# Performance work log

Hardware: AMD Instinct MI355X
Metric: run time of the kernel (lower is better)

Reference implementation:

```python
import jax, jax.numpy as jnp
import numpy as np

C = 64            # x_channel (d_model)
D = 2 * C         # d_inner (expand=2)
N = C // 2        # d_state
K = 4             # scan directions
R = -(-C // 16)   # dt_rank = ceil(d_model/16)
Bsz, H, W = 2, 48, 48
EPS = 1e-5


def setup_inputs() -> dict:
    key = jax.random.key(0)
    ks = jax.random.split(key, 8)
    g = lambda k, shp, s: jax.random.normal(k, shp, dtype=jnp.float32) * s
    return {
        "fufea1": g(ks[0], (Bsz, C, H, W), 1.0),
        "ln_g": jnp.ones((C,), jnp.float32),
        "ln_b": jnp.zeros((C,), jnp.float32),
        "in_proj_w": g(ks[1], (2 * D, C), C ** -0.5),
        "conv_w": g(ks[2], (D, 1, 3, 3), 1.0 / 3.0),   # depthwise 3x3
        "conv_b": g(ks[3], (D,), 0.02),
        "x_proj_w": g(ks[4], (K, R + 2 * N, D), D ** -0.5),
        "dt_w": g(ks[5], (K, D, R), R ** -0.5),
        "dt_b": g(ks[6], (K, D), 0.1),
        "A_logs": jnp.log(jnp.tile(jnp.arange(1, N + 1, dtype=jnp.float32), (K, D, 1))),  # S4D-real init
        "Ds": jnp.ones((K, D), jnp.float32),
        "out_ln_g": jnp.ones((D,), jnp.float32),
        "out_ln_b": jnp.zeros((D,), jnp.float32),
        "out_proj_w": g(ks[7], (C, D), D ** -0.5),
    }


def _layernorm(x, g, b):
    mu = x.mean(-1, keepdims=True)
    var = ((x - mu) ** 2).mean(-1, keepdims=True)
    return (x - mu) * jax.lax.rsqrt(var + EPS) * g + b


def reference(fufea1, ln_g, ln_b, in_proj_w, conv_w, conv_b, x_proj_w,
              dt_w, dt_b, A_logs, Ds, out_ln_g, out_ln_b, out_proj_w):
    B, Cc, Hh, Ww = fufea1.shape
    L = Hh * Ww
    # pre-LN (over channels, channels-last)
    xn = _layernorm(fufea1.transpose(0, 2, 3, 1), ln_g, ln_b)          # (B,H,W,C)
    # SS2D: in_proj -> split x,z
    xz = xn @ in_proj_w.T                                               # (B,H,W,2D)
    x, z = jnp.split(xz, 2, axis=-1)
    x = x.transpose(0, 3, 1, 2)                                         # (B,D,H,W)
    x = jax.lax.conv_general_dilated(x, conv_w, (1, 1), "SAME",
                                     feature_group_count=D,
                                     dimension_numbers=("NCHW", "OIHW", "NCHW"))
    x = jax.nn.silu(x + conv_b[None, :, None, None])
    # 4-direction sequences: row-major, col-major, and their reverses
    x_hw = x.reshape(B, D, L)
    x_wh = x.transpose(0, 1, 3, 2).reshape(B, D, L)
    xs = jnp.stack([x_hw, x_wh], axis=1)                                # (B,2,D,L)
    xs = jnp.concatenate([xs, jnp.flip(xs, axis=-1)], axis=1)           # (B,K,D,L)
    # per-direction projections of dt, B, C
    x_dbl = jnp.einsum("bkdl,kcd->bkcl", xs, x_proj_w)
    dts, Bs, Cs = jnp.split(x_dbl, [R, R + N], axis=2)                  # (B,K,R,L),(B,K,N,L),(B,K,N,L)
    dts = jnp.einsum("bkrl,kdr->bkdl", dts, dt_w)
    delta = jax.nn.softplus(dts + dt_b[None, :, :, None])               # (B,K,D,L)
    A = -jnp.exp(A_logs)                                                # (K,D,N)
    # selective scan over L; carry h: (B,K,D,N)
    u_l = xs.transpose(3, 0, 1, 2)                                      # (L,B,K,D)
    dt_l = delta.transpose(3, 0, 1, 2)
    B_l = Bs.transpose(3, 0, 1, 2)                                      # (L,B,K,N)
    C_l = Cs.transpose(3, 0, 1, 2)

    def step(h, inp):
        u_t, d_t, b_t, c_t = inp
        dA = jnp.exp(d_t[..., None] * A)                                # (B,K,D,N)
        h = dA * h + (d_t * u_t)[..., None] * b_t[:, :, None, :]
        y = jnp.einsum("bkdn,bkn->bkd", h, c_t)
        return h, y

    h0 = jnp.zeros((B, K, D, N), xs.dtype)
    _, ys = jax.lax.scan(step, h0, (u_l, dt_l, B_l, C_l))               # ys: (L,B,K,D)
    out_y = ys.transpose(1, 2, 3, 0) + Ds[None, :, :, None] * xs        # (B,K,D,L)
    # merge the 4 directions back to row-major hw order
    inv_y = jnp.flip(out_y[:, 2:4], axis=-1)                            # (B,2,D,L)
    wh = lambda t: t.reshape(B, D, Ww, Hh).transpose(0, 1, 3, 2).reshape(B, D, L)
    y = out_y[:, 0] + inv_y[:, 0] + wh(out_y[:, 1]) + wh(inv_y[:, 1])   # (B,D,L)
    y = y.transpose(0, 2, 1).reshape(B, Hh, Ww, D)
    y = _layernorm(y, out_ln_g, out_ln_b) * jax.nn.silu(z)
    out = (y @ out_proj_w.T).transpose(0, 3, 1, 2) + fufea1             # residual add
    return out
```

## Files before the change

### kernel.cpp

```cpp
#include <hip/hip_runtime.h>

#define Cc 64
#define Dd 128
#define Nn 32
#define Kk 4
#define Rr 4
#define Bb 2
#define Hh 48
#define Ww 48
#define Ll 2304
#define EPSf 1e-5f
#define LCc 144

#if __has_builtin(__builtin_amdgcn_exp2f)
#define EXP2F __builtin_amdgcn_exp2f
#else
#define EXP2F exp2f
#endif

__device__ __forceinline__ float wsum64(float v) {
  v += __shfl_xor(v, 32);
  v += __shfl_xor(v, 16);
  v += __shfl_xor(v, 8);
  v += __shfl_xor(v, 4);
  v += __shfl_xor(v, 2);
  v += __shfl_xor(v, 1);
  return v;
}

__device__ __forceinline__ float hmax32(float v) {
  v = fmaxf(v, __shfl_xor(v, 1));
  v = fmaxf(v, __shfl_xor(v, 2));
  v = fmaxf(v, __shfl_xor(v, 4));
  v = fmaxf(v, __shfl_xor(v, 8));
  v = fmaxf(v, __shfl_xor(v, 16));
  return v;
}

__device__ __forceinline__ int pixbase(int j, int k) {
  if (k == 0) return j;
  if (k == 2) return Ll - 1 - j;
  if (k == 1) return (j % Hh) * Ww + (j / Hh);
  const int jr = Ll - 1 - j;
  return (jr % Hh) * Ww + (jr / Hh);
}

__global__ __launch_bounds__(256) void k1_ln_inproj(
    const float* __restrict__ x, const float* __restrict__ g,
    const float* __restrict__ bta, const float* __restrict__ Wp,
    float* __restrict__ xin, float* __restrict__ zb)
{
  __shared__ float xS[16][65];
  __shared__ float xnS[16][64];
  const int tid = threadIdx.x;
  const int wv = tid >> 6, lane = tid & 63;
  const int pbase = blockIdx.x * 16;
  const int b = pbase / Ll;
  const int lbase = pbase % Ll;
  {
    const int c = tid >> 2, li0 = (tid & 3) * 4;
    const float4 v4 = *(const float4*)&x[(b * Cc + c) * Ll + lbase + li0];
    xS[li0 + 0][c] = v4.x;
    xS[li0 + 1][c] = v4.y;
    xS[li0 + 2][c] = v4.z;
    xS[li0 + 3][c] = v4.w;
  }
  __syncthreads();
  const float gv = g[lane], bv = bta[lane];
  for (int pi = 0; pi < 4; ++pi) {
    const int p = wv * 4 + pi;
    const float v = xS[p][lane];
    const float mu = wsum64(v) * (1.0f / 64.0f);
    const float dv = v - mu;
    const float var = wsum64(dv * dv) * (1.0f / 64.0f);
    const float rs = rsqrtf(var + EPSf);
    xnS[p][lane] = dv * rs * gv + bv;
  }
  __syncthreads();
  float acc[4][4];
  #pragma unroll
  for (int pi = 0; pi < 4; ++pi)
    #pragma unroll
    for (int m = 0; m < 4; ++m) acc[pi][m] = 0.f;
  const float4* W4 = (const float4*)Wp;
  #pragma unroll 4
  for (int c4 = 0; c4 < 16; ++c4) {
    float4 xn4[4];
    #pragma unroll
    for (int pi = 0; pi < 4; ++pi)
      xn4[pi] = ((const float4*)xnS[wv * 4 + pi])[c4];
    #pragma unroll
    for (int m = 0; m < 4; ++m) {
      const float4 w4 = W4[(lane + 64 * m) * 16 + c4];
      #pragma unroll
      for (int pi = 0; pi < 4; ++pi)
        acc[pi][m] += xn4[pi].x * w4.x + xn4[pi].y * w4.y +
                      xn4[pi].z * w4.z + xn4[pi].w * w4.w;
    }
  }
  #pragma unroll
  for (int pi = 0; pi < 4; ++pi) {
    const int l = lbase + wv * 4 + pi;
    const size_t base = (size_t)(b * Ll + l) * Dd;
    xin[base + lane]      = acc[pi][0];
    xin[base + lane + 64] = acc[pi][1];
    zb[base + lane]       = acc[pi][2];
    zb[base + lane + 64]  = acc[pi][3];
  }
}

__global__ __launch_bounds__(512) void k3_proj(
    const float* __restrict__ xin, const float* __restrict__ cw,
    const float* __restrict__ cb, const float* __restrict__ xpw,
    const float* __restrict__ dtw, const float* __restrict__ dtb,
    float* __restrict__ xc, float2* __restrict__ dd2,
    float* __restrict__ Bm, float* __restrict__ Cm)
{
  __shared__ float xinS[30][128];
  __shared__ float xvS[8][132];
  __shared__ float dtsS[8][16];
  const int t = threadIdx.x;
  const int pb = blockIdx.x * 8;
  const int b = pb / Ll;
  const int lb = pb % Ll;
  const int h0 = lb / Ww, w0 = lb % Ww;
  for (int i = t; i < 960; i += 512) {
    const int j = i >> 5, d4 = i & 31;
    const int r = j / 10, c = j % 10;
    const int hh = h0 + r - 1, ww = w0 + c - 1;
    float4 v = make_float4(0.f, 0.f, 0.f, 0.f);
    if (hh >= 0 && hh < Hh && ww >= 0 && ww < Ww)
      v = *(const float4*)&xin[((size_t)(b * Ll) + hh * Ww + ww) * Dd + d4 * 4];
    *(float4*)&xinS[j][d4 * 4] = v;
  }
  __syncthreads();
  for (int i = t; i < 1024; i += 512) {
    const int pi = i >> 7, d = i & 127;
    float acc = cb[d];
    #pragma unroll
    for (int r = 0; r < 3; ++r)
      #pragma unroll
      for (int c = 0; c < 3; ++c)
        acc += xinS[r * 10 + pi + c][d] * cw[d * 9 + r * 3 + c];
    const float sig = 1.0f / (1.0f + __expf(-acc));
    xvS[pi][d] = acc * sig;
  }
  __syncthreads();
  if (t < 272) {
    const int k = t / 68, c = t % 68;
    const size_t bkL = (size_t)(b * Kk + k) * Ll;
    float acc[8];
    #pragma unroll
    for (int pi = 0; pi < 8; ++pi) acc[pi] = 0.f;
    const float4* w4p = (const float4*)(xpw + (k * 68 + c) * 128);
    for (int d4 = 0; d4 < 32; ++d4) {
      const float4 w4 = w4p[d4];
      #pragma unroll
      for (int pi = 0; pi < 8; ++pi) {
        const float4 x4 = ((const float4*)xvS[pi])[d4];
        acc[pi] += x4.x * w4.x + x4.y * w4.y + x4.z * w4.z + x4.w * w4.w;
      }
    }
    #pragma unroll
    for (int pi = 0; pi < 8; ++pi) {
      const int l0 = lb + pi;
      const int h = l0 / Ww, w = l0 % Ww;
      int lk;
      if      (k == 0) lk = l0;
      else if (k == 1) lk = w * Hh + h;
      else if (k == 2) lk = Ll - 1 - l0;
      else             lk = Ll - 1 - (w * Hh + h);
      if (c < Rr)            dtsS[pi][k * 4 + c] = acc[pi];
      else if (c < Rr + Nn)  Bm[(bkL + lk) * Nn + (c - Rr)] = acc[pi];
      else                   Cm[(bkL + lk) * Nn + (c - Rr - Nn)] = acc[pi];
    }
  } else {
    for (int i = t - 272; i < 1024; i += 240) {
      const int pi = i >> 7, d = i & 127;
      xc[((size_t)(b * Ll) + lb + pi) * Dd + d] = xvS[pi][d];
    }
  }
  __syncthreads();
  {
    const int k = t >> 7, dd = t & 127;
    const float4 dw = *(const float4*)&dtw[(k * Dd + dd) * 4];
    const float biasv = dtb[k * Dd + dd];
    float2* drow = dd2 + ((size_t)((b * Kk + k) * Dd) + dd) * Ll;
    float2 buf[8];
    #pragma unroll
    for (int pi = 0; pi < 8; ++pi) {
      const float a = biasv
          + dtsS[pi][k * 4 + 0] * dw.x + dtsS[pi][k * 4 + 1] * dw.y
          + dtsS[pi][k * 4 + 2] * dw.z + dtsS[pi][k * 4 + 3] * dw.w;
      const float sp = (a > 20.f) ? a : log1pf(__expf(a));
      buf[pi] = make_float2(sp, sp * xvS[pi][dd]);
    }
    float4* f4 = (float4*)(drow + lb);
    #pragma unroll
    for (int j = 0; j < 4; ++j)
      f4[j] = make_float4(buf[2 * j].x, buf[2 * j].y, buf[2 * j + 1].x, buf[2 * j + 1].y);
  }
}

__global__ __launch_bounds__(512) void k4_scan(
    const float2* __restrict__ dd2, const float* __restrict__ Bm,
    const float* __restrict__ Cm, const float* __restrict__ Alogs,
    float* __restrict__ ys)
{
  __shared__ float2 ddS[Ll];
  __shared__ float hcS[16][32];
  __shared__ float sumDS[16];
  __shared__ float cmaxS[16];
  __shared__ float pS[16][8][36];
  const int tid = threadIdx.x;
  const int s = tid >> 5, n = tid & 31;
  const int blk = blockIdx.x;
  const int bk = blk & 7;
  const int d = blk >> 3;
  const int b = bk >> 2, k = bk & 3;
  const float An = -__expf(Alogs[(k * Dd + d) * Nn + n]);
  const float AnE = An * 1.44269504f;
  const size_t bkL = (size_t)(b * Kk + k) * Ll;
  const float2* dP = dd2 + ((size_t)((b * Kk + k) * Dd) + d) * Ll;
  const float* bP = Bm + bkL * Nn + n;
  const float* cP = Cm + bkL * Nn + n;
  const int lbeg = s * LCc;
  float* yD = ys + ((size_t)((b * Kk + k) * Dd) + d) * Ll;
  const int pstr = (k == 0) ? 1 : (k == 1) ? Ww : (k == 2) ? -1 : -Ww;
  const int rrow = n & 7, qtr = n >> 3;

  {
    const float4* src = (const float4*)dP;
    float4* dst = (float4*)ddS;
    #pragma unroll
    for (int i = 0; i < 3; ++i) {
      const int idx = tid + i * 512;
      if (idx < Ll / 2) dst[idx] = src[idx];
    }
  }
  __syncthreads();

  float h = 0.f, sumD = 0.f, cmx = 0.f;
  {
    const float* bl = bP + (size_t)lbeg * Nn;
    const float* cl = cP + (size_t)lbeg * Nn;
    float b0 = bl[0], b1 = bl[Nn], b2 = bl[2 * Nn], b3 = bl[3 * Nn];
    float c0 = cl[0], c1 = cl[Nn], c2 = cl[2 * Nn], c3 = cl[3 * Nn];
    int pb = pixbase(lbeg, k);
    float2 q0 = ddS[pb], q1 = ddS[pb + pstr], q2 = ddS[pb + 2 * pstr], q3 = ddS[pb + 3 * pstr];
    for (int t8 = 0; t8 < LCc / 8; ++t8) {
      const int j0n = lbeg + t8 * 8 + 8;
      const int pbn = pixbase(j0n <= Ll - 8 ? j0n : Ll - 8, k);
      #pragma unroll
      for (int half = 0; half < 2; ++half) {
        bl += 4 * Nn; cl += 4 * Nn;
        const int gb = (half == 0) ? pb + 4 * pstr : pbn;
        const float2 qn0 = ddS[gb], qn1 = ddS[gb + pstr],
                     qn2 = ddS[gb + 2 * pstr], qn3 = ddS[gb + 3 * pstr];
        const float b0n = bl[0], b1n = bl[Nn], b2n = bl[2 * Nn], b3n = bl[3 * Nn];
        const float c0n = cl[0], c1n = cl[Nn], c2n = cl[2 * Nn], c3n = cl[3 * Nn];
        h = EXP2F(q0.x * AnE) * h + q0.y * b0; pS[s][half * 4 + 0][n] = h * c0;
        h = EXP2F(q1.x * AnE) * h + q1.y * b1; pS[s][half * 4 + 1][n] = h * c1;
        h = EXP2F(q2.x * AnE) * h + q2.y * b2; pS[s][half * 4 + 2][n] = h * c2;
        h = EXP2F(q3.x * AnE) * h + q3.y * b3; pS[s][half * 4 + 3][n] = h * c3;
        sumD += (q0.x + q1.x) + (q2.x + q3.x);
        cmx = fmaxf(cmx, fmaxf(fmaxf(fabsf(c0), fabsf(c1)),
                               fmaxf(fabsf(c2), fabsf(c3))));
        q0 = qn0; q1 = qn1; q2 = qn2; q3 = qn3;
        b0 = b0n; b1 = b1n; b2 = b2n; b3 = b3n;
        c0 = c0n; c1 = c1n; c2 = c2n; c3 = c3n;
      }
      const float4 a4 = *(const float4*)&pS[s][rrow][qtr * 8];
      const float4 d4v = *(const float4*)&pS[s][rrow][qtr * 8 + 4];
      float sum = ((a4.x + a4.y) + (a4.z + a4.w)) + ((d4v.x + d4v.y) + (d4v.z + d4v.w));
      sum += __shfl_xor(sum, 8);
      sum += __shfl_xor(sum, 16);
      if (n < 8) yD[pb + n * pstr] = sum;
      pb = pbn;
    }
  }
  hcS[s][n] = h;
  const float cmxAll = hmax32(cmx);
  if (n == 0) { sumDS[s] = sumD; cmaxS[s] = cmxAll; }
  __syncthreads();
  if (tid < 32) {
    float carry = 0.f;
    #pragma unroll
    for (int s2 = 0; s2 < 16; ++s2) {
      const float hend = hcS[s2][tid];
      hcS[s2][tid] = carry;
      carry = EXP2F(AnE * sumDS[s2]) * carry + hend;
    }
  }
  __syncthreads();
  const float carry = hcS[s][n];
  const float mc = hmax32(fabsf(carry));
  const float AmaxE = hmax32(AnE);
  const float Pstop = log2f(mc * cmaxS[s] * 3.2e6f) / (-AmaxE);
  {
    float hc = carry, P = 0.f;
    const float* cl = cP + (size_t)lbeg * Nn;
    for (int t8 = 0; t8 < LCc / 8; ++t8) {
      if (!(P < Pstop)) break;
      const int pb = pixbase(lbeg + t8 * 8, k);
      #pragma unroll
      for (int half = 0; half < 2; ++half) {
        const int gb = pb + half * 4 * pstr;
        const float2 qq0 = ddS[gb], qq1 = ddS[gb + pstr],
                     qq2 = ddS[gb + 2 * pstr], qq3 = ddS[gb + 3 * pstr];
        hc *= EXP2F(qq0.x * AnE); pS[s][half * 4 + 0][n] = hc * cl[0];
        hc *= EXP2F(qq1.x * AnE); pS[s][half * 4 + 1][n] = hc * cl[Nn];
        hc *= EXP2F(qq2.x * AnE); pS[s][half * 4 + 2][n] = hc * cl[2 * Nn];
        hc *= EXP2F(qq3.x * AnE); pS[s][half * 4 + 3][n] = hc * cl[3 * Nn];
        P += (qq0.x + qq1.x) + (qq2.x + qq3.x);
        cl += 4 * Nn;
      }
      const float4 a4 = *(const float4*)&pS[s][rrow][qtr * 8];
      const float4 d4v = *(const float4*)&pS[s][rrow][qtr * 8 + 4];
      float sum = ((a4.x + a4.y) + (a4.z + a4.w)) + ((d4v.x + d4v.y) + (d4v.z + d4v.w));
      sum += __shfl_xor(sum, 8);
      sum += __shfl_xor(sum, 16);
      if (n < 8) yD[pb + n * pstr] += sum;
    }
  }
}

__global__ __launch_bounds__(256) void k5_merge(
    const float* __restrict__ ys, const float* __restrict__ zb,
    const float* __restrict__ og, const float* __restrict__ ob,
    const float* __restrict__ Wo, const float* __restrict__ resid,
    const float* __restrict__ xc, const float* __restrict__ DsP,
    float* __restrict__ out)
{
  __shared__ float ysS[16][132];
  __shared__ float xcS[16][128];
  __shared__ float tS[16][128];
  __shared__ float oS[64][17];
  const int tid = threadIdx.x;
  const int wv = tid >> 6, lane = tid & 63;
  const int pbase = blockIdx.x * 16;
  const int b = pbase / Ll;
  const int lbase = pbase % Ll;
  {
    const int li0 = (tid & 3) * 4, dh = tid >> 2;
    #pragma unroll
    for (int it = 0; it < 2; ++it) {
      const int d = dh + 64 * it;
      float4 acc = make_float4(0.f, 0.f, 0.f, 0.f);
      #pragma unroll
      for (int k = 0; k < 4; ++k) {
        const float4 v = *(const float4*)&ys[((size_t)(b * Kk + k) * Dd + d) * Ll + lbase + li0];
        acc.x += v.x; acc.y += v.y; acc.z += v.z; acc.w += v.w;
      }
      ysS[li0 + 0][d] = acc.x; ysS[li0 + 1][d] = acc.y;
      ysS[li0 + 2][d] = acc.z; ysS[li0 + 3][d] = acc.w;
    }
  }
  {
    const int p = tid >> 4, q = tid & 15;
    const float4* src = (const float4*)&xc[((size_t)(b * Ll) + lbase + p) * Dd];
    ((float4*)xcS[p])[q]      = src[q];
    ((float4*)xcS[p])[q + 16] = src[q + 16];
  }
  float sDs[2];
  #pragma unroll
  for (int m = 0; m < 2; ++m) {
    const int dch = lane + 64 * m;
    sDs[m] = DsP[dch] + DsP[Dd + dch] + DsP[2 * Dd + dch] + DsP[3 * Dd + dch];
  }
  __syncthreads();
  for (int pi = 0; pi < 4; ++pi) {
    const int p = wv * 4 + pi;
    const int l0 = lbase + p;
    float tv[2];
    #pragma unroll
    for (int m = 0; m < 2; ++m) {
      const int dch = lane + 64 * m;
      tv[m] = ysS[p][dch] + sDs[m] * xcS[p][dch];
    }
    const float mu = wsum64(tv[0] + tv[1]) * (1.0f / 128.0f);
    const float q = wsum64((tv[0] - mu) * (tv[0] - mu) +
                           (tv[1] - mu) * (tv[1] - mu)) * (1.0f / 128.0f);
    const float rs = rsqrtf(q + EPSf);
    #pragma unroll
    for (int m = 0; m < 2; ++m) {
      const int dch = lane + 64 * m;
      const float zz = zb[(size_t)(b * Ll + l0) * Dd + dch];
      const float sig = 1.0f / (1.0f + __expf(-zz));
      tS[p][dch] = ((tv[m] - mu) * rs * og[dch] + ob[dch]) * (zz * sig);
    }
  }
  __syncthreads();
  float acc[4] = {0.f, 0.f, 0.f, 0.f};
  const float4* W4 = (const float4*)Wo;
  for (int d4 = 0; d4 < 32; ++d4) {
    const float4 w4 = W4[lane * 32 + d4];
    #pragma unroll
    for (int pi = 0; pi < 4; ++pi) {
      const float4 t4 = ((const float4*)tS[wv * 4 + pi])[d4];
      acc[pi] += t4.x * w4.x + t4.y * w4.y + t4.z * w4.z + t4.w * w4.w;
    }
  }
  #pragma unroll
  for (int pi = 0; pi < 4; ++pi) oS[lane][wv * 4 + pi] = acc[pi];
  __syncthreads();
  const int c = tid >> 2, off = (tid & 3) * 4;
  const size_t obase = (size_t)(b * Cc + c) * Ll + lbase + off;
  const float4 r4 = *(const float4*)(resid + obase);
  float4 o4;
  o4.x = oS[c][off + 0] + r4.x;
  o4.y = oS[c][off + 1] + r4.y;
  o4.z = oS[c][off + 2] + r4.z;
  o4.w = oS[c][off + 3] + r4.w;
  *(float4*)(out + obase) = o4;
}

extern "C" void kernel_launch(void* const* d_in, const int* in_sizes, int n_in,
                              void* d_out, int out_size, void* d_ws, size_t ws_size,
                              hipStream_t stream)
{
  (void)in_sizes; (void)n_in; (void)out_size; (void)ws_size;
  const float* fufea1     = (const float*)d_in[0];
  const float* ln_g       = (const float*)d_in[1];
  const float* ln_b       = (const float*)d_in[2];
  const float* in_proj_w  = (const float*)d_in[3];
  const float* conv_w     = (const float*)d_in[4];
  const float* conv_b     = (const float*)d_in[5];
  const float* x_proj_w   = (const float*)d_in[6];
  const float* dt_w       = (const float*)d_in[7];
  const float* dt_b       = (const float*)d_in[8];
  const float* A_logs     = (const float*)d_in[9];
  const float* Ds         = (const float*)d_in[10];
  const float* out_ln_g   = (const float*)d_in[11];
  const float* out_ln_b   = (const float*)d_in[12];
  const float* out_proj_w = (const float*)d_in[13];

  float* ws = (float*)d_ws;
  float2* dd2 = (float2*)ws;
  float* Bm   = ws + 4718592;
  float* Cm   = ws + 5308416;
  float* zb   = ws + 5898240;
  float* xc   = ws + 6488064;
  float* ysb  = ws + 7077888;
  float* xin  = ws + 7077888;

  k1_ln_inproj<<<288, 256, 0, stream>>>(fufea1, ln_g, ln_b, in_proj_w, xin, zb);
  k3_proj<<<576, 512, 0, stream>>>(xin, conv_w, conv_b, x_proj_w, dt_w, dt_b,
                                   xc, dd2, Bm, Cm);
  k4_scan<<<1024, 512, 0, stream>>>(dd2, Bm, Cm, A_logs, ysb);
  k5_merge<<<288, 256, 0, stream>>>(ysb, zb, out_ln_g, out_ln_b, out_proj_w, fufea1,
                                    xc, Ds, (float*)d_out);
}
```

Before: 186.6 us.

## Fuse LayerNorm and in_proj into conv/projection kernel with halo recompute

Removes the separate LN+in_proj kernel and computes LayerNorm and the x-half of in_proj inside the conv/x_proj kernel for a 3x10 halo tile, writing z only for the 8 interior pixels. This drops one kernel launch and the global round-trip of the x-half activation buffer. The cost is recomputing the projection for halo pixels (about 3.75x redundant work on that half) and strided, uncoalesced per-channel input reads.

```diff
diff --git a/kernel.cpp b/kernel.cpp
--- a/kernel.cpp
+++ b/kernel.cpp
@@ -45,77 +45,17 @@
   return (jr % Hh) * Ww + (jr / Hh);
 }
 
-__global__ __launch_bounds__(256) void k1_ln_inproj(
+__global__ __launch_bounds__(512) void k3_proj(
     const float* __restrict__ x, const float* __restrict__ g,
     const float* __restrict__ bta, const float* __restrict__ Wp,
-    float* __restrict__ xin, float* __restrict__ zb)
-{
-  __shared__ float xS[16][65];
-  __shared__ float xnS[16][64];
-  const int tid = threadIdx.x;
-  const int wv = tid >> 6, lane = tid & 63;
-  const int pbase = blockIdx.x * 16;
-  const int b = pbase / Ll;
-  const int lbase = pbase % Ll;
-  {
-    const int c = tid >> 2, li0 = (tid & 3) * 4;
-    const float4 v4 = *(const float4*)&x[(b * Cc + c) * Ll + lbase + li0];
-    xS[li0 + 0][c] = v4.x;
-    xS[li0 + 1][c] = v4.y;
-    xS[li0 + 2][c] = v4.z;
-    xS[li0 + 3][c] = v4.w;
-  }
-  __syncthreads();
-  const float gv = g[lane], bv = bta[lane];
-  for (int pi = 0; pi < 4; ++pi) {
-    const int p = wv * 4 + pi;
-    const float v = xS[p][lane];
-    const float mu = wsum64(v) * (1.0f / 64.0f);
-    const float dv = v - mu;
-    const float var = wsum64(dv * dv) * (1.0f / 64.0f);
-    const float rs = rsqrtf(var + EPSf);
-    xnS[p][lane] = dv * rs * gv + bv;
-  }
-  __syncthreads();
-  float acc[4][4];
-  #pragma unroll
-  for (int pi = 0; pi < 4; ++pi)
-    #pragma unroll
-    for (int m = 0; m < 4; ++m) acc[pi][m] = 0.f;
-  const float4* W4 = (const float4*)Wp;
-  #pragma unroll 4
-  for (int c4 = 0; c4 < 16; ++c4) {
-    float4 xn4[4];
-    #pragma unroll
-    for (int pi = 0; pi < 4; ++pi)
-      xn4[pi] = ((const float4*)xnS[wv * 4 + pi])[c4];
-    #pragma unroll
-    for (int m = 0; m < 4; ++m) {
-      const float4 w4 = W4[(lane + 64 * m) * 16 + c4];
-      #pragma unroll
-      for (int pi = 0; pi < 4; ++pi)
-        acc[pi][m] += xn4[pi].x * w4.x + xn4[pi].y * w4.y +
-                      xn4[pi].z * w4.z + xn4[pi].w * w4.w;
-    }
-  }
-  #pragma unroll
-  for (int pi = 0; pi < 4; ++pi) {
-    const int l = lbase + wv * 4 + pi;
-    const size_t base = (size_t)(b * Ll + l) * Dd;
-    xin[base + lane]      = acc[pi][0];
-    xin[base + lane + 64] = acc[pi][1];
-    zb[base + lane]       = acc[pi][2];
-    zb[base + lane + 64]  = acc[pi][3];
-  }
-}
-
-__global__ __launch_bounds__(512) void k3_proj(
-    const float* __restrict__ xin, const float* __restrict__ cw,
-    const float* __restrict__ cb, const float* __restrict__ xpw,
-    const float* __restrict__ dtw, const float* __restrict__ dtb,
+    const float* __restrict__ cw, const float* __restrict__ cb,
+    const float* __restrict__ xpw, const float* __restrict__ dtw,
+    const float* __restrict__ dtb, float* __restrict__ zb,
     float* __restrict__ xc, float2* __restrict__ dd2,
     float* __restrict__ Bm, float* __restrict__ Cm)
 {
+  __shared__ float xS[30][65];
+  __shared__ float xnS[30][64];
   __shared__ float xinS[30][128];
   __shared__ float xvS[8][132];
   __shared__ float dtsS[8][16];
@@ -124,14 +64,70 @@
   const int b = pb / Ll;
   const int lb = pb % Ll;
   const int h0 = lb / Ww, w0 = lb % Ww;
-  for (int i = t; i < 960; i += 512) {
-    const int j = i >> 5, d4 = i & 31;
-    const int r = j / 10, c = j % 10;
-    const int hh = h0 + r - 1, ww = w0 + c - 1;
-    float4 v = make_float4(0.f, 0.f, 0.f, 0.f);
+  for (int idx = t; idx < 1920; idx += 512) {
+    const int c = idx / 30, j = idx % 30;
+    const int r = j / 10, col = j % 10;
+    const int hh = h0 + r - 1, ww = w0 + col - 1;
+    float v = 0.f;
     if (hh >= 0 && hh < Hh && ww >= 0 && ww < Ww)
-      v = *(const float4*)&xin[((size_t)(b * Ll) + hh * Ww + ww) * Dd + d4 * 4];
-    *(float4*)&xinS[j][d4 * 4] = v;
+      v = x[(b * Cc + c) * Ll + hh * Ww + ww];
+    xS[j][c] = v;
+  }
+  __syncthreads();
+  {
+    const int wv = t >> 6, lane = t & 63;
+    const float gv = g[lane], bv = bta[lane];
+    for (int pi = 0; pi < 4; ++pi) {
+      const int p = wv * 4 + pi;
+      if (p < 30) {
+        const float v = xS[p][lane];
+        const float mu = wsum64(v) * (1.0f / 64.0f);
+        const float dv = v - mu;
+        const float var = wsum64(dv * dv) * (1.0f / 64.0f);
+        const float rs = rsqrtf(var + EPSf);
+        xnS[p][lane] = dv * rs * gv + bv;
+      }
+    }
+  }
+  __syncthreads();
+  {
+    const int d = t & 127, pg = t >> 7;
+    float acc[8] = {0.f, 0.f, 0.f, 0.f, 0.f, 0.f, 0.f, 0.f};
+    const float4* Wr = (const float4*)(Wp + d * Cc);
+    for (int c4 = 0; c4 < 16; ++c4) {
+      const float4 w4 = Wr[c4];
+      #pragma unroll
+      for (int i = 0; i < 8; ++i) {
+        const int j = pg * 8 + i;
+        if (j < 30) {
+          const float4 xn4 = ((const float4*)xnS[j])[c4];
+          acc[i] += xn4.x * w4.x + xn4.y * w4.y + xn4.z * w4.z + xn4.w * w4.w;
+        }
+      }
+    }
+    #pragma unroll
+    for (int i = 0; i < 8; ++i) {
+      const int j = pg * 8 + i;
+      if (j < 30) {
+        const int r = j / 10, col = j % 10;
+        const int hh = h0 + r - 1, ww = w0 + col - 1;
+        const bool ok = (hh >= 0 && hh < Hh && ww >= 0 && ww < Ww);
+        xinS[j][d] = ok ? acc[i] : 0.f;
+      }
+    }
+    const float4* Wz = (const float4*)(Wp + (Dd + d) * Cc);
+    float accz[2] = {0.f, 0.f};
+    for (int c4 = 0; c4 < 16; ++c4) {
+      const float4 w4 = Wz[c4];
+      #pragma unroll
+      for (int i = 0; i < 2; ++i) {
+        const float4 xn4 = ((const float4*)xnS[11 + pg * 2 + i])[c4];
+        accz[i] += xn4.x * w4.x + xn4.y * w4.y + xn4.z * w4.z + xn4.w * w4.w;
+      }
+    }
+    #pragma unroll
+    for (int i = 0; i < 2; ++i)
+      zb[((size_t)(b * Ll) + lb + pg * 2 + i) * Dd + d] = accz[i];
   }
   __syncthreads();
   for (int i = t; i < 1024; i += 512) {
@@ -442,11 +438,9 @@
   float* zb   = ws + 5898240;
   float* xc   = ws + 6488064;
   float* ysb  = ws + 7077888;
-  float* xin  = ws + 7077888;
-
-  k1_ln_inproj<<<288, 256, 0, stream>>>(fufea1, ln_g, ln_b, in_proj_w, xin, zb);
-  k3_proj<<<576, 512, 0, stream>>>(xin, conv_w, conv_b, x_proj_w, dt_w, dt_b,
-                                   xc, dd2, Bm, Cm);
+
+  k3_proj<<<576, 512, 0, stream>>>(fufea1, ln_g, ln_b, in_proj_w, conv_w, conv_b,
+                                   x_proj_w, dt_w, dt_b, zb, xc, dd2, Bm, Cm);
   k4_scan<<<1024, 512, 0, stream>>>(dd2, Bm, Cm, A_logs, ysb);
   k5_merge<<<288, 256, 0, stream>>>(ysb, zb, out_ln_g, out_ln_b, out_proj_w, fufea1,
                                     xc, Ds, (float*)d_out);
```

Measured after the change: 196.5 us. 5.3% more time.

## Process two d-channels per scan block to reuse B/C loads

Applied to the files above, without the earlier changes.

Each scan block now handles two adjacent inner channels, loading both channels' delta/u rows into shared memory and running two interleaved recurrences. The B and C values read from global memory are shared between the two channels, which halves that traffic and gives each thread two independent dependency chains for more instruction-level parallelism. The cost is half as many blocks (512), roughly double the shared memory per block and more registers, so occupancy may drop. The early-exit in the carry-correction pass now runs until both channels reach their stop threshold.

```diff
diff --git a/kernel.cpp b/kernel.cpp
--- a/kernel.cpp
+++ b/kernel.cpp
@@ -207,47 +207,53 @@
     const float* __restrict__ Cm, const float* __restrict__ Alogs,
     float* __restrict__ ys)
 {
-  __shared__ float2 ddS[Ll];
-  __shared__ float hcS[16][32];
-  __shared__ float sumDS[16];
+  __shared__ float2 ddS[2][Ll];
+  __shared__ float hcS[2][16][32];
+  __shared__ float sumDS[2][16];
   __shared__ float cmaxS[16];
-  __shared__ float pS[16][8][36];
+  __shared__ float pSA[16][8][36];
+  __shared__ float pSB[16][8][36];
   const int tid = threadIdx.x;
   const int s = tid >> 5, n = tid & 31;
   const int blk = blockIdx.x;
   const int bk = blk & 7;
-  const int d = blk >> 3;
+  const int dp = blk >> 3;
+  const int d0 = dp * 2;
   const int b = bk >> 2, k = bk & 3;
-  const float An = -__expf(Alogs[(k * Dd + d) * Nn + n]);
-  const float AnE = An * 1.44269504f;
+  const float AnE0 = -__expf(Alogs[(k * Dd + d0) * Nn + n]) * 1.44269504f;
+  const float AnE1 = -__expf(Alogs[(k * Dd + d0 + 1) * Nn + n]) * 1.44269504f;
   const size_t bkL = (size_t)(b * Kk + k) * Ll;
-  const float2* dP = dd2 + ((size_t)((b * Kk + k) * Dd) + d) * Ll;
+  const float2* dP0 = dd2 + ((size_t)((b * Kk + k) * Dd) + d0) * Ll;
   const float* bP = Bm + bkL * Nn + n;
   const float* cP = Cm + bkL * Nn + n;
   const int lbeg = s * LCc;
-  float* yD = ys + ((size_t)((b * Kk + k) * Dd) + d) * Ll;
+  float* yD0 = ys + ((size_t)((b * Kk + k) * Dd) + d0) * Ll;
+  float* yD1 = yD0 + Ll;
   const int pstr = (k == 0) ? 1 : (k == 1) ? Ww : (k == 2) ? -1 : -Ww;
   const int rrow = n & 7, qtr = n >> 3;
 
   {
-    const float4* src = (const float4*)dP;
+    const float4* src = (const float4*)dP0;
     float4* dst = (float4*)ddS;
     #pragma unroll
-    for (int i = 0; i < 3; ++i) {
+    for (int i = 0; i < 5; ++i) {
       const int idx = tid + i * 512;
-      if (idx < Ll / 2) dst[idx] = src[idx];
-    }
-  }
-  __syncthreads();
-
-  float h = 0.f, sumD = 0.f, cmx = 0.f;
+      if (idx < Ll) dst[idx] = src[idx];
+    }
+  }
+  __syncthreads();
+
+  float h0 = 0.f, h1 = 0.f, sD0 = 0.f, sD1 = 0.f, cmx = 0.f;
   {
     const float* bl = bP + (size_t)lbeg * Nn;
     const float* cl = cP + (size_t)lbeg * Nn;
     float b0 = bl[0], b1 = bl[Nn], b2 = bl[2 * Nn], b3 = bl[3 * Nn];
     float c0 = cl[0], c1 = cl[Nn], c2 = cl[2 * Nn], c3 = cl[3 * Nn];
     int pb = pixbase(lbeg, k);
-    float2 q0 = ddS[pb], q1 = ddS[pb + pstr], q2 = ddS[pb + 2 * pstr], q3 = ddS[pb + 3 * pstr];
+    float2 qa0 = ddS[0][pb], qa1 = ddS[0][pb + pstr],
+           qa2 = ddS[0][pb + 2 * pstr], qa3 = ddS[0][pb + 3 * pstr];
+    float2 qb0 = ddS[1][pb], qb1 = ddS[1][pb + pstr],
+           qb2 = ddS[1][pb + 2 * pstr], qb3 = ddS[1][pb + 3 * pstr];
     for (int t8 = 0; t8 < LCc / 8; ++t8) {
       const int j0n = lbeg + t8 * 8 + 8;
       const int pbn = pixbase(j0n <= Ll - 8 ? j0n : Ll - 8, k);
@@ -255,72 +261,111 @@
       for (int half = 0; half < 2; ++half) {
         bl += 4 * Nn; cl += 4 * Nn;
         const int gb = (half == 0) ? pb + 4 * pstr : pbn;
-        const float2 qn0 = ddS[gb], qn1 = ddS[gb + pstr],
-                     qn2 = ddS[gb + 2 * pstr], qn3 = ddS[gb + 3 * pstr];
+        const float2 na0 = ddS[0][gb], na1 = ddS[0][gb + pstr],
+                     na2 = ddS[0][gb + 2 * pstr], na3 = ddS[0][gb + 3 * pstr];
+        const float2 nb0 = ddS[1][gb], nb1 = ddS[1][gb + pstr],
+                     nb2 = ddS[1][gb + 2 * pstr], nb3 = ddS[1][gb + 3 * pstr];
         const float b0n = bl[0], b1n = bl[Nn], b2n = bl[2 * Nn], b3n = bl[3 * Nn];
         const float c0n = cl[0], c1n = cl[Nn], c2n = cl[2 * Nn], c3n = cl[3 * Nn];
-        h = EXP2F(q0.x * AnE) * h + q0.y * b0; pS[s][half * 4 + 0][n] = h * c0;
-        h = EXP2F(q1.x * AnE) * h + q1.y * b1; pS[s][half * 4 + 1][n] = h * c1;
-        h = EXP2F(q2.x * AnE) * h + q2.y * b2; pS[s][half * 4 + 2][n] = h * c2;
-        h = EXP2F(q3.x * AnE) * h + q3.y * b3; pS[s][half * 4 + 3][n] = h * c3;
-        sumD += (q0.x + q1.x) + (q2.x + q3.x);
+        h0 = EXP2F(qa0.x * AnE0) * h0 + qa0.y * b0; pSA[s][half * 4 + 0][n] = h0 * c0;
+        h1 = EXP2F(qb0.x * AnE1) * h1 + qb0.y * b0; pSB[s][half * 4 + 0][n] = h1 * c0;
+        h0 = EXP2F(qa1.x * AnE0) * h0 + qa1.y * b1; pSA[s][half * 4 + 1][n] = h0 * c1;
+        h1 = EXP2F(qb1.x * AnE1) * h1 + qb1.y * b1; pSB[s][half * 4 + 1][n] = h1 * c1;
+        h0 = EXP2F(qa2.x * AnE0) * h0 + qa2.y * b2; pSA[s][half * 4 + 2][n] = h0 * c2;
+        h1 = EXP2F(qb2.x * AnE1) * h1 + qb2.y * b2; pSB[s][half * 4 + 2][n] = h1 * c2;
+        h0 = EXP2F(qa3.x * AnE0) * h0 + qa3.y * b3; pSA[s][half * 4 + 3][n] = h0 * c3;
+        h1 = EXP2F(qb3.x * AnE1) * h1 + qb3.y * b3; pSB[s][half * 4 + 3][n] = h1 * c3;
+        sD0 += (qa0.x + qa1.x) + (qa2.x + qa3.x);
+        sD1 += (qb0.x + qb1.x) + (qb2.x + qb3.x);
         cmx = fmaxf(cmx, fmaxf(fmaxf(fabsf(c0), fabsf(c1)),
                                fmaxf(fabsf(c2), fabsf(c3))));
-        q0 = qn0; q1 = qn1; q2 = qn2; q3 = qn3;
+        qa0 = na0; qa1 = na1; qa2 = na2; qa3 = na3;
+        qb0 = nb0; qb1 = nb1; qb2 = nb2; qb3 = nb3;
         b0 = b0n; b1 = b1n; b2 = b2n; b3 = b3n;
         c0 = c0n; c1 = c1n; c2 = c2n; c3 = c3n;
       }
-      const float4 a4 = *(const float4*)&pS[s][rrow][qtr * 8];
-      const float4 d4v = *(const float4*)&pS[s][rrow][qtr * 8 + 4];
-      float sum = ((a4.x + a4.y) + (a4.z + a4.w)) + ((d4v.x + d4v.y) + (d4v.z + d4v.w));
-      sum += __shfl_xor(sum, 8);
-      sum += __shfl_xor(sum, 16);
-      if (n < 8) yD[pb + n * pstr] = sum;
+      {
+        const float4 a4 = *(const float4*)&pSA[s][rrow][qtr * 8];
+        const float4 d4v = *(const float4*)&pSA[s][rrow][qtr * 8 + 4];
+        float sumA = ((a4.x + a4.y) + (a4.z + a4.w)) + ((d4v.x + d4v.y) + (d4v.z + d4v.w));
+        const float4 e4 = *(const float4*)&pSB[s][rrow][qtr * 8];
+        const float4 f4 = *(const float4*)&pSB[s][rrow][qtr * 8 + 4];
+        float sumB = ((e4.x + e4.y) + (e4.z + e4.w)) + ((f4.x + f4.y) + (f4.z + f4.w));
+        sumA += __shfl_xor(sumA, 8);
+        sumB += __shfl_xor(sumB, 8);
+        sumA += __shfl_xor(sumA, 16);
+        sumB += __shfl_xor(sumB, 16);
+        if (n < 8) {
+          yD0[pb + n * pstr] = sumA;
+          yD1[pb + n * pstr] = sumB;
+        }
+      }
       pb = pbn;
     }
   }
-  hcS[s][n] = h;
+  hcS[0][s][n] = h0;
+  hcS[1][s][n] = h1;
   const float cmxAll = hmax32(cmx);
-  if (n == 0) { sumDS[s] = sumD; cmaxS[s] = cmxAll; }
-  __syncthreads();
-  if (tid < 32) {
+  if (n == 0) { sumDS[0][s] = sD0; sumDS[1][s] = sD1; cmaxS[s] = cmxAll; }
+  __syncthreads();
+  if (tid < 64) {
+    const int ch = tid >> 5, ln = tid & 31;
+    const float AnE = (ch == 0) ? AnE0 : AnE1;
     float carry = 0.f;
     #pragma unroll
     for (int s2 = 0; s2 < 16; ++s2) {
-      const float hend = hcS[s2][tid];
-      hcS[s2][tid] = carry;
-      carry = EXP2F(AnE * sumDS[s2]) * carry + hend;
-    }
-  }
-  __syncthreads();
-  const float carry = hcS[s][n];
-  const float mc = hmax32(fabsf(carry));
-  const float AmaxE = hmax32(AnE);
-  const float Pstop = log2f(mc * cmaxS[s] * 3.2e6f) / (-AmaxE);
-  {
-    float hc = carry, P = 0.f;
+      const float hend = hcS[ch][s2][ln];
+      hcS[ch][s2][ln] = carry;
+      carry = EXP2F(AnE * sumDS[ch][s2]) * carry + hend;
+    }
+  }
+  __syncthreads();
+  const float carryA = hcS[0][s][n], carryB = hcS[1][s][n];
+  const float mcA = hmax32(fabsf(carryA));
+  const float mcB = hmax32(fabsf(carryB));
+  const float AmaxE0 = hmax32(AnE0);
+  const float AmaxE1 = hmax32(AnE1);
+  const float Pstop0 = log2f(mcA * cmaxS[s] * 3.2e6f) / (-AmaxE0);
+  const float Pstop1 = log2f(mcB * cmaxS[s] * 3.2e6f) / (-AmaxE1);
+  {
+    float hA = carryA, hB = carryB, P0 = 0.f, P1 = 0.f;
     const float* cl = cP + (size_t)lbeg * Nn;
     for (int t8 = 0; t8 < LCc / 8; ++t8) {
-      if (!(P < Pstop)) break;
+      if (!(P0 < Pstop0) && !(P1 < Pstop1)) break;
       const int pb = pixbase(lbeg + t8 * 8, k);
       #pragma unroll
       for (int half = 0; half < 2; ++half) {
         const int gb = pb + half * 4 * pstr;
-        const float2 qq0 = ddS[gb], qq1 = ddS[gb + pstr],
-                     qq2 = ddS[gb + 2 * pstr], qq3 = ddS[gb + 3 * pstr];
-        hc *= EXP2F(qq0.x * AnE); pS[s][half * 4 + 0][n] = hc * cl[0];
-        hc *= EXP2F(qq1.x * AnE); pS[s][half * 4 + 1][n] = hc * cl[Nn];
-        hc *= EXP2F(qq2.x * AnE); pS[s][half * 4 + 2][n] = hc * cl[2 * Nn];
-        hc *= EXP2F(qq3.x * AnE); pS[s][half * 4 + 3][n] = hc * cl[3 * Nn];
-        P += (qq0.x + qq1.x) + (qq2.x + qq3.x);
+        const float2 u0 = ddS[0][gb], u1 = ddS[0][gb + pstr],
+                     u2 = ddS[0][gb + 2 * pstr], u3 = ddS[0][gb + 3 * pstr];
+        const float2 v0 = ddS[1][gb], v1 = ddS[1][gb + pstr],
+                     v2 = ddS[1][gb + 2 * pstr], v3 = ddS[1][gb + 3 * pstr];
+        hA *= EXP2F(u0.x * AnE0); pSA[s][half * 4 + 0][n] = hA * cl[0];
+        hB *= EXP2F(v0.x * AnE1); pSB[s][half * 4 + 0][n] = hB * cl[0];
+        hA *= EXP2F(u1.x * AnE0); pSA[s][half * 4 + 1][n] = hA * cl[Nn];
+        hB *= EXP2F(v1.x * AnE1); pSB[s][half * 4 + 1][n] = hB * cl[Nn];
+        hA *= EXP2F(u2.x * AnE0); pSA[s][half * 4 + 2][n] = hA * cl[2 * Nn];
+        hB *= EXP2F(v2.x * AnE1); pSB[s][half * 4 + 2][n] = hB * cl[2 * Nn];
+        hA *= EXP2F(u3.x * AnE0); pSA[s][half * 4 + 3][n] = hA * cl[3 * Nn];
+        hB *= EXP2F(v3.x * AnE1); pSB[s][half * 4 + 3][n] = hB * cl[3 * Nn];
+        P0 += (u0.x + u1.x) + (u2.x + u3.x);
+        P1 += (v0.x + v1.x) + (v2.x + v3.x);
         cl += 4 * Nn;
       }
-      const float4 a4 = *(const float4*)&pS[s][rrow][qtr * 8];
-      const float4 d4v = *(const float4*)&pS[s][rrow][qtr * 8 + 4];
-      float sum = ((a4.x + a4.y) + (a4.z + a4.w)) + ((d4v.x + d4v.y) + (d4v.z + d4v.w));
-      sum += __shfl_xor(sum, 8);
-      sum += __shfl_xor(sum, 16);
-      if (n < 8) yD[pb + n * pstr] += sum;
+      const float4 a4 = *(const float4*)&pSA[s][rrow][qtr * 8];
+      const float4 d4v = *(const float4*)&pSA[s][rrow][qtr * 8 + 4];
+      float sumA = ((a4.x + a4.y) + (a4.z + a4.w)) + ((d4v.x + d4v.y) + (d4v.z + d4v.w));
+      const float4 e4 = *(const float4*)&pSB[s][rrow][qtr * 8];
+      const float4 f4 = *(const float4*)&pSB[s][rrow][qtr * 8 + 4];
+      float sumB = ((e4.x + e4.y) + (e4.z + e4.w)) + ((f4.x + f4.y) + (f4.z + f4.w));
+      sumA += __shfl_xor(sumA, 8);
+      sumB += __shfl_xor(sumB, 8);
+      sumA += __shfl_xor(sumA, 16);
+      sumB += __shfl_xor(sumB, 16);
+      if (n < 8) {
+        yD0[pb + n * pstr] += sumA;
+        yD1[pb + n * pstr] += sumB;
+      }
     }
   }
 }
@@ -447,7 +492,7 @@
   k1_ln_inproj<<<288, 256, 0, stream>>>(fufea1, ln_g, ln_b, in_proj_w, xin, zb);
   k3_proj<<<576, 512, 0, stream>>>(xin, conv_w, conv_b, x_proj_w, dt_w, dt_b,
                                    xc, dd2, Bm, Cm);
-  k4_scan<<<1024, 512, 0, stream>>>(dd2, Bm, Cm, A_logs, ysb);
+  k4_scan<<<512, 512, 0, stream>>>(dd2, Bm, Cm, A_logs, ysb);
   k5_merge<<<288, 256, 0, stream>>>(ysb, zb, out_ln_g, out_ln_b, out_proj_w, fufea1,
                                     xc, Ds, (float*)d_out);
 }
```

After: 186.7 us. No clear change (+0.0%).
